# Kernel optimization log

Measured on AMD Instinct MI355X. Metric: run time of the kernel, lower is better.

Reference implementation:

```python
import jax, jax.numpy as jnp
import numpy as np

N = 50000        # nodes
E = 1600000      # edges (before self-loops)
F_IN = 11        # QM9 node features
H = 128          # dim_h
G = 1024         # number of graphs in the mega-batch
T = 1            # targets_num


def setup_inputs() -> dict:
    key = jax.random.key(0)
    ks = jax.random.split(key, 8)
    x = jax.random.normal(ks[0], (N, F_IN), jnp.float32)
    edge_index = jax.random.randint(ks[1], (2, E), 0, N, dtype=jnp.int32)
    batch = jnp.sort(jax.random.randint(ks[2], (N,), 0, G, dtype=jnp.int32))
    W1 = jax.random.normal(ks[3], (F_IN, H), jnp.float32) / np.float32(np.sqrt(F_IN))
    b1 = jnp.zeros((H,), jnp.float32)
    W2 = jax.random.normal(ks[4], (H, H), jnp.float32) / np.float32(np.sqrt(H))
    b2 = jnp.zeros((H,), jnp.float32)
    W3 = jax.random.normal(ks[5], (H, H), jnp.float32) / np.float32(np.sqrt(H))
    b3 = jnp.zeros((H,), jnp.float32)
    Wl = jax.random.normal(ks[6], (H, T), jnp.float32) / np.float32(np.sqrt(H))
    bl = jnp.zeros((T,), jnp.float32)
    return {"x": x, "edge_index": edge_index, "batch": batch,
            "W1": W1, "b1": b1, "W2": W2, "b2": b2, "W3": W3, "b3": b3,
            "Wl": Wl, "bl": bl}


def gcn_conv(x, W, b, src, dst, norm, n):
    # PyG GCNConv: linear (no bias), normalized scatter-add over edges, then bias.
    h = x @ W                                  # [N, H]
    msg = h[src] * norm[:, None]               # [E+N, H] gather + scale
    agg = jax.ops.segment_sum(msg, dst, num_segments=n)
    return agg + b


def reference(x, edge_index, batch, W1, b1, W2, b2, W3, b3, Wl, bl):
    n = x.shape[0]
    loop = jnp.arange(n, dtype=edge_index.dtype)
    src = jnp.concatenate([edge_index[0], loop])   # self-loops added (PyG default)
    dst = jnp.concatenate([edge_index[1], loop])
    deg = jax.ops.segment_sum(jnp.ones_like(dst, jnp.float32), dst, num_segments=n)
    dinv = jnp.where(deg > 0, jax.lax.rsqrt(jnp.maximum(deg, 1.0)), 0.0)
    norm = dinv[src] * dinv[dst]                   # D^{-1/2}(A+I)D^{-1/2}

    h = jax.nn.relu(gcn_conv(x, W1, b1, src, dst, norm, n))
    h = jax.nn.relu(gcn_conv(h, W2, b2, src, dst, norm, n))
    h = gcn_conv(h, W3, b3, src, dst, norm, n)

    # global mean pool over graph segment ids
    g = batch.astype(jnp.int32)
    s = jax.ops.segment_sum(h, g, num_segments=G)
    cnt = jax.ops.segment_sum(jnp.ones((n, 1), jnp.float32), g, num_segments=G)
    pooled = s / jnp.maximum(cnt, 1.0)

    # dropout is identity at eval time (training=False)
    return pooled @ Wl + bl
```

## Files before the change

### kernel.cpp

```cpp
#include <hip/hip_runtime.h>
#include <hip/hip_fp16.h>


constexpr int N_NODES = 50000;
constexpr int N_EDGES = 1600000;
constexpr int F_IN_C  = 11;
constexpr int HC      = 128;
constexpr int G_C     = 1024;
constexpr int NPB     = 128;
constexpr int NB      = (N_NODES + NPB - 1) / NPB;
constexpr int CHUNK   = 8192;
constexpr int NBLK_E  = (N_EDGES + CHUNK - 1) / CHUNK;


__device__ __forceinline__ unsigned pack_f16(float x, float y) {
  __half2 h = __floats2half2_rn(x, y);
  return *reinterpret_cast<unsigned*>(&h);
}

__device__ __forceinline__ float2 unpack_f16(unsigned u) {
  __half2 h = *reinterpret_cast<__half2*>(&u);
  return __half22float2(h);
}


__global__ __launch_bounds__(256) void k_bhist(const int* __restrict__ dst,
                                               int* __restrict__ bcnt) {
  __shared__ int hist[NB];
  int t = threadIdx.x;
  for (int b = t; b < NB; b += 256) hist[b] = 0;
  __syncthreads();
  long e0 = (long)blockIdx.x * CHUNK;
  for (int it = 0; it < CHUNK / 1024; ++it) {
    long e = e0 + it * 1024 + t * 4;
    if (e < N_EDGES) {
      int4 d4 = *(const int4*)(dst + e);
      atomicAdd(&hist[d4.x >> 7], 1);
      atomicAdd(&hist[d4.y >> 7], 1);
      atomicAdd(&hist[d4.z >> 7], 1);
      atomicAdd(&hist[d4.w >> 7], 1);
    }
  }
  __syncthreads();
  for (int b = t; b < NB; b += 256)
    if (hist[b]) atomicAdd(&bcnt[b], hist[b]);
}

__global__ __launch_bounds__(512) void k_prefix(const int* __restrict__ bcnt,
                                                int* __restrict__ bbase,
                                                int* __restrict__ bcur) {
  __shared__ int sc[512];
  int t = threadIdx.x;
  int v = (t < NB) ? bcnt[t] : 0;
  sc[t] = v;
  __syncthreads();
  for (int off = 1; off < 512; off <<= 1) {
    int a = (t >= off) ? sc[t - off] : 0;
    __syncthreads();
    sc[t] += a;
    __syncthreads();
  }
  if (t < NB) {
    int excl = sc[t] - v;
    bbase[t] = excl;
    bcur[t]  = excl;
  }
}

__global__ __launch_bounds__(256) void k_bin(const int* __restrict__ src,
                                             const int* __restrict__ dst,
                                             int* __restrict__ bcur,
                                             unsigned int* __restrict__ pairs) {
  __shared__ int hist[NB], base[NB], loff[NB];
  int t = threadIdx.x;
  for (int b = t; b < NB; b += 256) { hist[b] = 0; loff[b] = 0; }
  __syncthreads();
  long e0 = (long)blockIdx.x * CHUNK;
  for (int it = 0; it < CHUNK / 1024; ++it) {
    long e = e0 + it * 1024 + t * 4;
    if (e < N_EDGES) {
      int4 d4 = *(const int4*)(dst + e);
      atomicAdd(&hist[d4.x >> 7], 1);
      atomicAdd(&hist[d4.y >> 7], 1);
      atomicAdd(&hist[d4.z >> 7], 1);
      atomicAdd(&hist[d4.w >> 7], 1);
    }
  }
  __syncthreads();
  for (int b = t; b < NB; b += 256)
    if (hist[b]) base[b] = atomicAdd(&bcur[b], hist[b]);
  __syncthreads();
  for (int it = 0; it < CHUNK / 1024; ++it) {
    long e = e0 + it * 1024 + t * 4;
    if (e < N_EDGES) {
      int4 s4 = *(const int4*)(src + e);
      int4 d4 = *(const int4*)(dst + e);
      {
        int b = d4.x >> 7;
        int l = atomicAdd(&loff[b], 1);
        pairs[base[b] + l] = (unsigned)s4.x | ((unsigned)(d4.x & 127) << 16);
      }
      {
        int b = d4.y >> 7;
        int l = atomicAdd(&loff[b], 1);
        pairs[base[b] + l] = (unsigned)s4.y | ((unsigned)(d4.y & 127) << 16);
      }
      {
        int b = d4.z >> 7;
        int l = atomicAdd(&loff[b], 1);
        pairs[base[b] + l] = (unsigned)s4.z | ((unsigned)(d4.z & 127) << 16);
      }
      {
        int b = d4.w >> 7;
        int l = atomicAdd(&loff[b], 1);
        pairs[base[b] + l] = (unsigned)s4.w | ((unsigned)(d4.w & 127) << 16);
      }
    }
  }
}

__global__ __launch_bounds__(256) void k_build(const unsigned int* __restrict__ pairs,
                                               const int* __restrict__ bbase,
                                               const int* __restrict__ bcur,
                                               int* __restrict__ total,
                                               int* __restrict__ start,
                                               int* __restrict__ deg,
                                               float* __restrict__ dinv,
                                               int* __restrict__ csr) {
  __shared__ int cntL[NPB], sc[NPB];
  __shared__ int csrBaseL;
  int t = threadIdx.x;
  int b = blockIdx.x;
  int nodeBase = b * NPB;
  int nib = min(NPB, N_NODES - nodeBase);
  int pbase = bbase[b];
  int pend  = bcur[b];
  int size  = pend - pbase;
  if (t < NPB) cntL[t] = 0;
  __syncthreads();
  for (int p = t; p < size; p += 256)
    atomicAdd(&cntL[pairs[pbase + p] >> 16], 1);
  __syncthreads();
  int d = 0;
  if (t < NPB) {
    d = (t < nib) ? cntL[t] + 1 : 0;
    sc[t] = d;
  }
  __syncthreads();
  for (int off = 1; off < NPB; off <<= 1) {
    int a = 0;
    if (t < NPB && t >= off) a = sc[t - off];
    __syncthreads();
    if (t < NPB) sc[t] += a;
    __syncthreads();
  }
  if (t == 0) csrBaseL = atomicAdd(total, sc[NPB - 1]);
  __syncthreads();
  int csrBase = csrBaseL;
  if (t < nib) {
    int excl = sc[t] - d;
    int n = nodeBase + t;
    int s = csrBase + excl;
    start[n] = s;
    deg[n]   = d;
    dinv[n]  = rsqrtf((float)d);
    csr[s]   = n;
    cntL[t]  = excl + 1;
  }
  __syncthreads();
  for (int p = t; p < size; p += 256) {
    unsigned v = pairs[pbase + p];
    int loc = atomicAdd(&cntL[v >> 16], 1);
    csr[csrBase + loc] = (int)(v & 0xFFFFu);
  }
}


__global__ __launch_bounds__(256) void k_lin1(const float* __restrict__ x,
                                              const float* __restrict__ W1,
                                              unsigned* __restrict__ out) {
  __shared__ float w_s[F_IN_C * HC];
  for (int i = threadIdx.x; i < F_IN_C * HC; i += 256) w_s[i] = W1[i];
  __syncthreads();
  int lane = threadIdx.x & 63;
  int sub  = threadIdx.x >> 6;
  for (int n = blockIdx.x * 4 + sub; n < N_NODES; n += gridDim.x * 4) {
    const float* xr = x + (size_t)n * F_IN_C;
    float ax = 0.f, ay = 0.f;
#pragma unroll
    for (int k = 0; k < F_IN_C; ++k) {
      float xv = xr[k];
      ax += xv * w_s[k * HC + 2 * lane];
      ay += xv * w_s[k * HC + 2 * lane + 1];
    }
    out[(size_t)n * 64 + lane] = pack_f16(ax, ay);
  }
}

__global__ __launch_bounds__(128) void k_gemm(const float* __restrict__ in,
                                              const float* __restrict__ W,
                                              unsigned* __restrict__ out) {
  __shared__ float in_s[16][HC];
  int t  = threadIdx.x;
  int n0 = blockIdx.x * 16;
#pragma unroll
  for (int r = 0; r < 16; ++r) in_s[r][t] = in[(size_t)(n0 + r) * HC + t];
  __syncthreads();
  int tp = t & 63;
  int rg = t >> 6;
  float accx[8], accy[8];
#pragma unroll
  for (int r = 0; r < 8; ++r) { accx[r] = 0.f; accy[r] = 0.f; }
  for (int k = 0; k < HC; ++k) {
    float2 w2 = *(const float2*)(W + k * HC + 2 * tp);
#pragma unroll
    for (int r = 0; r < 8; ++r) {
      float a = in_s[rg * 8 + r][k];
      accx[r] += a * w2.x;
      accy[r] += a * w2.y;
    }
  }
#pragma unroll
  for (int r = 0; r < 8; ++r)
    out[(size_t)(n0 + rg * 8 + r) * 64 + tp] = pack_f16(accx[r], accy[r]);
}

__global__ __launch_bounds__(128) void k_v3(const float* __restrict__ W3,
                                            const float* __restrict__ b3,
                                            const float* __restrict__ Wl,
                                            float* __restrict__ v3,
                                            float* __restrict__ c3) {
  int k = threadIdx.x;
  float acc = 0.f;
  for (int j = 0; j < HC; ++j) acc += W3[k * HC + j] * Wl[j];
  v3[k] = acc;
  __shared__ float red[128];
  red[k] = b3[k] * Wl[k];
  __syncthreads();
  for (int s = 64; s > 0; s >>= 1) {
    if (k < s) red[k] += red[k + s];
    __syncthreads();
  }
  if (k == 0) *c3 = red[0];
}


template <int MODE>
__global__ __launch_bounds__(256) void k_spmm(const unsigned* __restrict__ lin,
                                              const float* __restrict__ dinv,
                                              const int* __restrict__ start,
                                              const int* __restrict__ deg,
                                              const int* __restrict__ csr,
                                              const float* __restrict__ bias,
                                              const float* __restrict__ v3,
                                              float* __restrict__ out) {
  int wv = threadIdx.x >> 6, lane = threadIdx.x & 63;
  int n = blockIdx.x * 4 + wv;
  if (n >= N_NODES) return;
  int s0 = start[n], d = deg[n];
  float dn = dinv[n];
  float ax[8], ay[8];
#pragma unroll
  for (int u = 0; u < 8; ++u) { ax[u] = 0.f; ay[u] = 0.f; }
  int i = 0;
  for (; i + 8 <= d; i += 8) {
    int j[8];
    float w[8];
    unsigned q[8];
#pragma unroll
    for (int u = 0; u < 8; ++u) j[u] = csr[s0 + i + u];
#pragma unroll
    for (int u = 0; u < 8; ++u) w[u] = dinv[j[u]];
#pragma unroll
    for (int u = 0; u < 8; ++u) q[u] = lin[(size_t)j[u] * 64 + lane];
#pragma unroll
    for (int u = 0; u < 8; ++u) {
      float2 v = unpack_f16(q[u]);
      ax[u] += w[u] * v.x;
      ay[u] += w[u] * v.y;
    }
  }
  for (; i < d; ++i) {
    int j0 = csr[s0 + i];
    float w0 = dinv[j0];
    float2 v = unpack_f16(lin[(size_t)j0 * 64 + lane]);
    ax[0] += w0 * v.x;
    ay[0] += w0 * v.y;
  }
  float sx = ((ax[0] + ax[1]) + (ax[2] + ax[3])) + ((ax[4] + ax[5]) + (ax[6] + ax[7]));
  float sy = ((ay[0] + ay[1]) + (ay[2] + ay[3])) + ((ay[4] + ay[5]) + (ay[6] + ay[7]));
  sx = fmaxf(sx * dn + bias[lane * 2], 0.f);
  sy = fmaxf(sy * dn + bias[lane * 2 + 1], 0.f);
  if (MODE == 0) {
    ((float2*)out)[(size_t)n * 64 + lane] = make_float2(sx, sy);
  } else {
    float2 vv = ((const float2*)v3)[lane];
    float p = sx * vv.x + sy * vv.y;
#pragma unroll
    for (int o = 32; o > 0; o >>= 1) p += __shfl_down(p, o, 64);
    if (lane == 0) out[n] = p;
  }
}

__global__ __launch_bounds__(256) void k_spmv_pool(const float* __restrict__ t,
                                                   const float* __restrict__ dinv,
                                                   const int* __restrict__ start,
                                                   const int* __restrict__ deg,
                                                   const int* __restrict__ csr,
                                                   const float* __restrict__ c3,
                                                   const int* __restrict__ batch,
                                                   float* __restrict__ ssum,
                                                   int* __restrict__ cntg) {
  int n = blockIdx.x * 256 + threadIdx.x;
  if (n >= N_NODES) return;
  int s0 = start[n], d = deg[n];
  float a0 = 0.f, a1 = 0.f, a2 = 0.f, a3 = 0.f;
  int i = 0;
  for (; i + 4 <= d; i += 4) {
    int j0 = csr[s0 + i], j1 = csr[s0 + i + 1];
    int j2 = csr[s0 + i + 2], j3 = csr[s0 + i + 3];
    a0 += dinv[j0] * t[j0];
    a1 += dinv[j1] * t[j1];
    a2 += dinv[j2] * t[j2];
    a3 += dinv[j3] * t[j3];
  }
  for (; i < d; ++i) {
    int j0 = csr[s0 + i];
    a0 += dinv[j0] * t[j0];
  }
  float acc = ((a0 + a1) + (a2 + a3)) * dinv[n] + *c3;
  int g = batch[n];
  atomicAdd(&ssum[g], acc);
  atomicAdd(&cntg[g], 1);
}

__global__ __launch_bounds__(256) void k_out(const float* __restrict__ ssum,
                                             const int* __restrict__ cntg,
                                             const float* __restrict__ bl,
                                             float* __restrict__ out) {
  int g = blockIdx.x * 256 + threadIdx.x;
  if (g < G_C) out[g] = ssum[g] / fmaxf((float)cntg[g], 1.f) + bl[0];
}


extern "C" void kernel_launch(void* const* d_in, const int* in_sizes, int n_in,
                              void* d_out, int out_size, void* d_ws, size_t ws_size,
                              hipStream_t stream) {
  const float* x     = (const float*)d_in[0];
  const int*   ei    = (const int*)d_in[1];
  const int*   srcE  = ei;
  const int*   dstE  = ei + N_EDGES;
  const int*   batch = (const int*)d_in[2];
  const float* W1 = (const float*)d_in[3];
  const float* b1 = (const float*)d_in[4];
  const float* W2 = (const float*)d_in[5];
  const float* b2 = (const float*)d_in[6];
  const float* W3 = (const float*)d_in[7];
  const float* b3 = (const float*)d_in[8];
  const float* Wl = (const float*)d_in[9];
  const float* bl = (const float*)d_in[10];
  float* out = (float*)d_out;

  size_t off = 0;
  auto alloc = [&](size_t bytes) -> char* {
    char* p = (char*)d_ws + off;
    off = (off + bytes + 15) & ~(size_t)15;
    return p;
  };
  char* bufA = alloc((size_t)N_NODES * HC * 4);
  float* bufB = (float*)alloc((size_t)N_NODES * HC * 4);
  unsigned* pairs = (unsigned*)bufA;
  unsigned* lin1  = (unsigned*)bufA;
  unsigned* lin2  = (unsigned*)(bufA + (size_t)N_NODES * 64 * 4);
  float* dinv = (float*)alloc((size_t)N_NODES * 4);
  float* tbuf = (float*)alloc((size_t)N_NODES * 4);
  float* v3   = (float*)alloc(HC * 4);
  float* c3   = (float*)alloc(16);
  int* startA = (int*)alloc((size_t)N_NODES * 4);
  int* degA   = (int*)alloc((size_t)N_NODES * 4);
  int* csr    = (int*)alloc((size_t)(N_EDGES + N_NODES) * 4);
  int* bbase  = (int*)alloc(NB * 4);
  int* bcur   = (int*)alloc(NB * 4);
  size_t zz_bytes = NB * 4 + 16 + G_C * 4 + G_C * 4;
  char* zz = alloc(zz_bytes);
  int*   bcnt = (int*)zz;
  int*   total= (int*)(zz + NB * 4);
  float* ssum = (float*)(zz + NB * 4 + 16);
  int*   cntg = (int*)(zz + NB * 4 + 16 + G_C * 4);

  hipMemsetAsync(zz, 0, zz_bytes, stream);

  k_bhist<<<NBLK_E, 256, 0, stream>>>(dstE, bcnt);
  k_prefix<<<1, 512, 0, stream>>>(bcnt, bbase, bcur);
  k_bin<<<NBLK_E, 256, 0, stream>>>(srcE, dstE, bcur, pairs);
  k_build<<<NB, 256, 0, stream>>>(pairs, bbase, bcur, total, startA, degA, dinv, csr);
  k_v3<<<1, 128, 0, stream>>>(W3, b3, Wl, v3, c3);

  k_lin1<<<N_NODES / 4, 256, 0, stream>>>(x, W1, lin1);
  k_spmm<0><<<N_NODES / 4, 256, 0, stream>>>(lin1, dinv, startA, degA, csr, b1, v3, bufB);
  k_gemm<<<N_NODES / 16, 128, 0, stream>>>(bufB, W2, lin2);
  k_spmm<1><<<N_NODES / 4, 256, 0, stream>>>(lin2, dinv, startA, degA, csr, b2, v3, tbuf);
  k_spmv_pool<<<(N_NODES + 255) / 256, 256, 0, stream>>>(tbuf, dinv, startA, degA, csr,
                                                         c3, batch, ssum, cntg);
  k_out<<<(G_C + 255) / 256, 256, 0, stream>>>(ssum, cntg, bl, out);
}
```

Before: 275.6 us.

## Prescale features by dinv and pad CSR rows to multiples of 8 with zero row

Folds the source-side D^-1/2 scaling into the producers (lin1, gemm, and the spmm<1> output), so the gather loops no longer load dinv[j] per edge. CSR rows are padded to a multiple of 8 with a sentinel index that points at a zeroed extra feature row. This lets the SpMM and SpMV loops use aligned int4 index loads with no scalar tail. The cost is extra padded gathers of the zero row, which add up to about 7 per node, plus larger CSR and feature buffers. The layout now depends on the sentinel rows being zeroed in k_v3 before use.

```diff
diff --git a/kernel.cpp b/kernel.cpp
--- a/kernel.cpp
+++ b/kernel.cpp
@@ -11,6 +11,7 @@
 constexpr int NB      = (N_NODES + NPB - 1) / NPB;
 constexpr int CHUNK   = 8192;
 constexpr int NBLK_E  = (N_EDGES + CHUNK - 1) / CHUNK;
+constexpr int ZROW    = N_NODES;
 
 
 __device__ __forceinline__ unsigned pack_f16(float x, float y) {
@@ -141,11 +142,12 @@
   for (int p = t; p < size; p += 256)
     atomicAdd(&cntL[pairs[pbase + p] >> 16], 1);
   __syncthreads();
-  int d = 0;
-  if (t < NPB) {
-    d = (t < nib) ? cntL[t] + 1 : 0;
-    sc[t] = d;
-  }
+  int d = 0, dpad = 0;
+  if (t < NPB && t < nib) {
+    d = cntL[t] + 1;
+    dpad = (d + 7) & ~7;
+  }
+  if (t < NPB) sc[t] = dpad;
   __syncthreads();
   for (int off = 1; off < NPB; off <<= 1) {
     int a = 0;
@@ -158,13 +160,14 @@
   __syncthreads();
   int csrBase = csrBaseL;
   if (t < nib) {
-    int excl = sc[t] - d;
+    int excl = sc[t] - dpad;
     int n = nodeBase + t;
     int s = csrBase + excl;
     start[n] = s;
-    deg[n]   = d;
+    deg[n]   = dpad;
     dinv[n]  = rsqrtf((float)d);
     csr[s]   = n;
+    for (int k = d; k < dpad; ++k) csr[s + k] = ZROW;
     cntL[t]  = excl + 1;
   }
   __syncthreads();
@@ -178,6 +181,7 @@
 
 __global__ __launch_bounds__(256) void k_lin1(const float* __restrict__ x,
                                               const float* __restrict__ W1,
+                                              const float* __restrict__ dinv,
                                               unsigned* __restrict__ out) {
   __shared__ float w_s[F_IN_C * HC];
   for (int i = threadIdx.x; i < F_IN_C * HC; i += 256) w_s[i] = W1[i];
@@ -193,12 +197,14 @@
       ax += xv * w_s[k * HC + 2 * lane];
       ay += xv * w_s[k * HC + 2 * lane + 1];
     }
-    out[(size_t)n * 64 + lane] = pack_f16(ax, ay);
+    float dn = dinv[n];
+    out[(size_t)n * 64 + lane] = pack_f16(ax * dn, ay * dn);
   }
 }
 
 __global__ __launch_bounds__(128) void k_gemm(const float* __restrict__ in,
                                               const float* __restrict__ W,
+                                              const float* __restrict__ dinv,
                                               unsigned* __restrict__ out) {
   __shared__ float in_s[16][HC];
   int t  = threadIdx.x;
@@ -221,19 +227,30 @@
     }
   }
 #pragma unroll
-  for (int r = 0; r < 8; ++r)
-    out[(size_t)(n0 + rg * 8 + r) * 64 + tp] = pack_f16(accx[r], accy[r]);
+  for (int r = 0; r < 8; ++r) {
+    int n = n0 + rg * 8 + r;
+    float dn = dinv[n];
+    out[(size_t)n * 64 + tp] = pack_f16(accx[r] * dn, accy[r] * dn);
+  }
 }
 
 __global__ __launch_bounds__(128) void k_v3(const float* __restrict__ W3,
                                             const float* __restrict__ b3,
                                             const float* __restrict__ Wl,
                                             float* __restrict__ v3,
-                                            float* __restrict__ c3) {
+                                            float* __restrict__ c3,
+                                            unsigned* __restrict__ lin1,
+                                            unsigned* __restrict__ lin2,
+                                            float* __restrict__ tbuf) {
   int k = threadIdx.x;
   float acc = 0.f;
   for (int j = 0; j < HC; ++j) acc += W3[k * HC + j] * Wl[j];
   v3[k] = acc;
+  if (k < 64) {
+    lin1[(size_t)ZROW * 64 + k] = 0u;
+    lin2[(size_t)ZROW * 64 + k] = 0u;
+  }
+  if (k == 64) tbuf[ZROW] = 0.f;
   __shared__ float red[128];
   red[k] = b3[k] * Wl[k];
   __syncthreads();
@@ -263,29 +280,53 @@
 #pragma unroll
   for (int u = 0; u < 8; ++u) { ax[u] = 0.f; ay[u] = 0.f; }
   int i = 0;
-  for (; i + 8 <= d; i += 8) {
-    int j[8];
-    float w[8];
+  for (; i + 16 <= d; i += 16) {
+    int4 c0 = *(const int4*)(csr + s0 + i);
+    int4 c1 = *(const int4*)(csr + s0 + i + 4);
+    int4 c2 = *(const int4*)(csr + s0 + i + 8);
+    int4 c3i = *(const int4*)(csr + s0 + i + 12);
+    unsigned q[16];
+    q[0]  = lin[(size_t)c0.x * 64 + lane];
+    q[1]  = lin[(size_t)c0.y * 64 + lane];
+    q[2]  = lin[(size_t)c0.z * 64 + lane];
+    q[3]  = lin[(size_t)c0.w * 64 + lane];
+    q[4]  = lin[(size_t)c1.x * 64 + lane];
+    q[5]  = lin[(size_t)c1.y * 64 + lane];
+    q[6]  = lin[(size_t)c1.z * 64 + lane];
+    q[7]  = lin[(size_t)c1.w * 64 + lane];
+    q[8]  = lin[(size_t)c2.x * 64 + lane];
+    q[9]  = lin[(size_t)c2.y * 64 + lane];
+    q[10] = lin[(size_t)c2.z * 64 + lane];
+    q[11] = lin[(size_t)c2.w * 64 + lane];
+    q[12] = lin[(size_t)c3i.x * 64 + lane];
+    q[13] = lin[(size_t)c3i.y * 64 + lane];
+    q[14] = lin[(size_t)c3i.z * 64 + lane];
+    q[15] = lin[(size_t)c3i.w * 64 + lane];
+#pragma unroll
+    for (int u = 0; u < 16; ++u) {
+      float2 v = unpack_f16(q[u]);
+      ax[u & 7] += v.x;
+      ay[u & 7] += v.y;
+    }
+  }
+  if (i < d) {
+    int4 c0 = *(const int4*)(csr + s0 + i);
+    int4 c1 = *(const int4*)(csr + s0 + i + 4);
     unsigned q[8];
-#pragma unroll
-    for (int u = 0; u < 8; ++u) j[u] = csr[s0 + i + u];
-#pragma unroll
-    for (int u = 0; u < 8; ++u) w[u] = dinv[j[u]];
-#pragma unroll
-    for (int u = 0; u < 8; ++u) q[u] = lin[(size_t)j[u] * 64 + lane];
+    q[0] = lin[(size_t)c0.x * 64 + lane];
+    q[1] = lin[(size_t)c0.y * 64 + lane];
+    q[2] = lin[(size_t)c0.z * 64 + lane];
+    q[3] = lin[(size_t)c0.w * 64 + lane];
+    q[4] = lin[(size_t)c1.x * 64 + lane];
+    q[5] = lin[(size_t)c1.y * 64 + lane];
+    q[6] = lin[(size_t)c1.z * 64 + lane];
+    q[7] = lin[(size_t)c1.w * 64 + lane];
 #pragma unroll
     for (int u = 0; u < 8; ++u) {
       float2 v = unpack_f16(q[u]);
-      ax[u] += w[u] * v.x;
-      ay[u] += w[u] * v.y;
-    }
-  }
-  for (; i < d; ++i) {
-    int j0 = csr[s0 + i];
-    float w0 = dinv[j0];
-    float2 v = unpack_f16(lin[(size_t)j0 * 64 + lane]);
-    ax[0] += w0 * v.x;
-    ay[0] += w0 * v.y;
+      ax[u] += v.x;
+      ay[u] += v.y;
+    }
   }
   float sx = ((ax[0] + ax[1]) + (ax[2] + ax[3])) + ((ax[4] + ax[5]) + (ax[6] + ax[7]));
   float sy = ((ay[0] + ay[1]) + (ay[2] + ay[3])) + ((ay[4] + ay[5]) + (ay[6] + ay[7]));
@@ -298,7 +339,7 @@
     float p = sx * vv.x + sy * vv.y;
 #pragma unroll
     for (int o = 32; o > 0; o >>= 1) p += __shfl_down(p, o, 64);
-    if (lane == 0) out[n] = p;
+    if (lane == 0) out[n] = p * dn;
   }
 }
 
@@ -315,18 +356,12 @@
   if (n >= N_NODES) return;
   int s0 = start[n], d = deg[n];
   float a0 = 0.f, a1 = 0.f, a2 = 0.f, a3 = 0.f;
-  int i = 0;
-  for (; i + 4 <= d; i += 4) {
-    int j0 = csr[s0 + i], j1 = csr[s0 + i + 1];
-    int j2 = csr[s0 + i + 2], j3 = csr[s0 + i + 3];
-    a0 += dinv[j0] * t[j0];
-    a1 += dinv[j1] * t[j1];
-    a2 += dinv[j2] * t[j2];
-    a3 += dinv[j3] * t[j3];
-  }
-  for (; i < d; ++i) {
-    int j0 = csr[s0 + i];
-    a0 += dinv[j0] * t[j0];
+  for (int i = 0; i + 4 <= d; i += 4) {
+    int4 c = *(const int4*)(csr + s0 + i);
+    a0 += t[c.x];
+    a1 += t[c.y];
+    a2 += t[c.z];
+    a3 += t[c.w];
   }
   float acc = ((a0 + a1) + (a2 + a3)) * dinv[n] + *c3;
   int g = batch[n];
@@ -367,18 +402,18 @@
     off = (off + bytes + 15) & ~(size_t)15;
     return p;
   };
-  char* bufA = alloc((size_t)N_NODES * HC * 4);
+  char* bufA = alloc((size_t)(N_NODES + 1) * 2 * 256);
   float* bufB = (float*)alloc((size_t)N_NODES * HC * 4);
   unsigned* pairs = (unsigned*)bufA;
   unsigned* lin1  = (unsigned*)bufA;
-  unsigned* lin2  = (unsigned*)(bufA + (size_t)N_NODES * 64 * 4);
+  unsigned* lin2  = (unsigned*)(bufA + (size_t)(N_NODES + 1) * 256);
   float* dinv = (float*)alloc((size_t)N_NODES * 4);
-  float* tbuf = (float*)alloc((size_t)N_NODES * 4);
+  float* tbuf = (float*)alloc((size_t)(N_NODES + 1) * 4);
   float* v3   = (float*)alloc(HC * 4);
   float* c3   = (float*)alloc(16);
   int* startA = (int*)alloc((size_t)N_NODES * 4);
   int* degA   = (int*)alloc((size_t)N_NODES * 4);
-  int* csr    = (int*)alloc((size_t)(N_EDGES + N_NODES) * 4);
+  int* csr    = (int*)alloc((size_t)(N_EDGES + 8 * N_NODES) * 4);
   int* bbase  = (int*)alloc(NB * 4);
   int* bcur   = (int*)alloc(NB * 4);
   size_t zz_bytes = NB * 4 + 16 + G_C * 4 + G_C * 4;
@@ -394,11 +429,11 @@
   k_prefix<<<1, 512, 0, stream>>>(bcnt, bbase, bcur);
   k_bin<<<NBLK_E, 256, 0, stream>>>(srcE, dstE, bcur, pairs);
   k_build<<<NB, 256, 0, stream>>>(pairs, bbase, bcur, total, startA, degA, dinv, csr);
-  k_v3<<<1, 128, 0, stream>>>(W3, b3, Wl, v3, c3);
-
-  k_lin1<<<N_NODES / 4, 256, 0, stream>>>(x, W1, lin1);
+  k_v3<<<1, 128, 0, stream>>>(W3, b3, Wl, v3, c3, lin1, lin2, tbuf);
+
+  k_lin1<<<N_NODES / 4, 256, 0, stream>>>(x, W1, dinv, lin1);
   k_spmm<0><<<N_NODES / 4, 256, 0, stream>>>(lin1, dinv, startA, degA, csr, b1, v3, bufB);
-  k_gemm<<<N_NODES / 16, 128, 0, stream>>>(bufB, W2, lin2);
+  k_gemm<<<N_NODES / 16, 128, 0, stream>>>(bufB, W2, dinv, lin2);
   k_spmm<1><<<N_NODES / 4, 256, 0, stream>>>(lin2, dinv, startA, degA, csr, b2, v3, tbuf);
   k_spmv_pool<<<(N_NODES + 255) / 256, 256, 0, stream>>>(tbuf, dinv, startA, degA, csr,
                                                          c3, batch, ssum, cntg);
```

New measurement: 245.1 us. -11.1%, faster.
